# Kernel tuning notes

Hardware: AMD Instinct MI355X
Metric: run time of the kernel (lower is better)

Reference implementation:

```python
import jax, jax.numpy as jnp
import numpy as np

# Static graph-batch geometry: B graphs, N nodes each (contiguous), DEG avg degree.
B, N, DEG = 128, 512, 16
GID, GH = 128, 128      # g_in_dim, g_hidden_dim
CID, CE = 64, 64        # c_in_dim, c_embed_dim
HAZ = 256               # haz_dim
K1, K2, K3 = 256, 128, 64


def _gcn(x, src, dst, mask, W, b, n):
    # GCN layer with self loops over masked (surviving) nodes; masked-out nodes contribute nothing.
    h = x @ W  # [n, GH]
    w = mask[src] * mask[dst]                                  # edge alive iff both endpoints alive
    deg = mask + jax.ops.segment_sum(w, dst, num_segments=n)    # +mask = self loop
    dinv = jax.lax.rsqrt(jnp.maximum(deg, 1.0))
    norm = w * dinv[src] * dinv[dst]
    agg = jax.ops.segment_sum(norm[:, None] * h[src], dst, num_segments=n)
    self_term = h * (mask * dinv * dinv)[:, None]               # self-loop norm = 1/deg
    return (agg + self_term + b) * mask[:, None]


def _pool(x, mask, p, k):
    # Score-based top-k pooling (MVPool score -> gate -> keep top ratio per graph), mask-based for static shapes.
    score = jax.nn.sigmoid((x @ p) / jnp.sqrt(jnp.sum(p * p)))  # [B*N]
    s = jnp.where(mask > 0, score, -jnp.inf).reshape(B, N)
    _, idx = jax.lax.top_k(s, k)                                 # [B, k]
    new_mask = jnp.zeros((B, N), x.dtype).at[jnp.arange(B)[:, None], idx].set(1.0).reshape(-1)
    x = x * (score * new_mask)[:, None]
    return x, new_mask


def _readout(x, mask):
    # readout='both': concat(global_max_pool, global_mean_pool) per graph.
    xm = x.reshape(B, N, -1)
    m = mask.reshape(B, N, 1)
    mx = jnp.max(jnp.where(m > 0, xm, -1e30), axis=1)
    avg = jnp.sum(xm * m, axis=1) / jnp.maximum(jnp.sum(m, axis=1), 1.0)
    return jnp.concatenate([mx, avg], axis=1)


def _forward(x, inp_c, src, dst, W1, b1, W2, b2, W3, b3, p1, p2, p3, We, Wa, ba, Wb, bb, Wc):
    n = B * N
    mask = jnp.ones((n,), x.dtype)
    x = jax.nn.relu(_gcn(x, src, dst, mask, W1, b1, n))
    x, mask = _pool(x, mask, p1, K1)
    x1 = _readout(x, mask)
    x = jax.nn.relu(_gcn(x, src, dst, mask, W2, b2, n))
    x, mask = _pool(x, mask, p2, K2)
    x2 = _readout(x, mask)
    x = jax.nn.relu(_gcn(x, src, dst, mask, W3, b3, n))
    x, mask = _pool(x, mask, p3, K3)
    x3 = _readout(x, mask)
    hg = jax.nn.relu(x1) + jax.nn.relu(x2) + jax.nn.relu(x3)     # [B, 2*GH]
    embed = jax.nn.relu(inp_c @ We)                               # [B, CE]
    fusion = jnp.concatenate([embed, hg], axis=1)                 # [B, 320]
    h = jax.nn.relu(fusion @ Wa + ba)                             # dropout skipped (eval mode)
    h = jax.nn.relu(h @ Wb + bb)
    return h @ Wc                                                 # out_dim=1 -> Identity


def setup_inputs() -> dict:
    key = jax.random.key(0)
    ks = jax.random.split(key, 16)
    n = B * N
    x = jax.random.normal(ks[0], (n, GID), jnp.float32)
    inp_c = jax.random.normal(ks[1], (B, CID), jnp.float32)
    offs = (jnp.arange(B, dtype=jnp.int32) * N)[:, None]
    src = (jax.random.randint(ks[2], (B, N * DEG), 0, N, jnp.int32) + offs).reshape(-1)
    dst = (jax.random.randint(ks[3], (B, N * DEG), 0, N, jnp.int32) + offs).reshape(-1)
    edge_index = jnp.stack([src, dst])
    batch = jnp.arange(n, dtype=jnp.int32) // N
    def lin(k, i, o):
        return jax.random.normal(k, (i, o), jnp.float32) / np.float32(np.sqrt(i))
    return dict(
        x=x, inp_c=inp_c, edge_index=edge_index, batch=batch,
        W1=lin(ks[4], GID, GH), b1=jnp.zeros((GH,), jnp.float32),
        W2=lin(ks[5], GH, GH), b2=jnp.zeros((GH,), jnp.float32),
        W3=lin(ks[6], GH, GH), b3=jnp.zeros((GH,), jnp.float32),
        p1=jax.random.normal(ks[7], (GH,), jnp.float32),
        p2=jax.random.normal(ks[8], (GH,), jnp.float32),
        p3=jax.random.normal(ks[9], (GH,), jnp.float32),
        We=lin(ks[10], CID, CE),
        Wa=lin(ks[11], 2 * GH + CE, HAZ), ba=jnp.zeros((HAZ,), jnp.float32),
        Wb=lin(ks[12], HAZ, HAZ // 2), bb=jnp.zeros((HAZ // 2,), jnp.float32),
        Wc=lin(ks[13], HAZ // 2, 1),
    )


def reference(x, inp_c, edge_index, batch, W1, b1, W2, b2, W3, b3, p1, p2, p3, We, Wa, ba, Wb, bb, Wc):
    # batch is implicitly arange(n)//N (contiguous equal-size graphs); reductions use the reshape form.
    src, dst = edge_index[0], edge_index[1]
    return _forward(x, inp_c, src, dst, W1, b1, W2, b2, W3, b3, p1, p2, p3, We, Wa, ba, Wb, bb, Wc)
```

## Files before the change

### kernel.cpp

```cpp
#include <hip/hip_runtime.h>
#include <math.h>

#define NNODE 65536
#define NEDGE 1048576
#define NGRAPH 128
#define NPG 512
#define EPG 8192

typedef _Float16 f16x8 __attribute__((ext_vector_type(8)));
typedef _Float16 f16x4 __attribute__((ext_vector_type(4)));
typedef float f32x4 __attribute__((ext_vector_type(4)));


__global__ __launch_bounds__(512) void k_csr(const int* __restrict__ srcE, const int* __restrict__ dstE,
                                             int* __restrict__ rp, int* __restrict__ csr,
                                             float* __restrict__ gate, int* __restrict__ alive,
                                             float* __restrict__ dinv) {
    __shared__ int cnt[512];
    __shared__ int tmp[512];
    int g = blockIdx.x, t = threadIdx.x;
    int nd = g * NPG + t;
    cnt[t] = 0;
    gate[nd] = 1.f;
    alive[nd] = nd;
    __syncthreads();
    int ebase = g * EPG;
    int dl[16];
    for (int i = 0; i < 16; ++i) {
        int e = ebase + t + i * 512;
        int d = dstE[e] - g * NPG;
        dl[i] = d;
        atomicAdd(&cnt[d], 1);
    }
    __syncthreads();
    int v = cnt[t], incl = v;
    dinv[nd] = rsqrtf(1.f + (float)v);
    for (int off = 1; off < 512; off <<= 1) {
        tmp[t] = incl; __syncthreads();
        if (t >= off) incl += tmp[t - off];
        __syncthreads();
    }
    int excl = incl - v;
    rp[nd] = ebase + excl;
    if (g == NGRAPH - 1 && t == 511) rp[NNODE] = NEDGE;
    __syncthreads();
    cnt[t] = excl;
    __syncthreads();
    for (int i = 0; i < 16; ++i) {
        int e = ebase + t + i * 512;
        int pos = atomicAdd(&cnt[dl[i]], 1);
        csr[ebase + pos] = srcE[e];
    }
}


__global__ __launch_bounds__(256) void k_wconv(const float* __restrict__ W0, const float* __restrict__ W1,
                                               const float* __restrict__ W2, _Float16* __restrict__ wh,
                                               _Float16* __restrict__ wl) {
    int l = blockIdx.x >> 6;
    int e = (blockIdx.x & 63) * 256 + threadIdx.x;
    const float* W = (l == 0) ? W0 : (l == 1) ? W1 : W2;
    int k = e >> 7, n = e & 127;
    float w = W[e];
    _Float16 hi = (_Float16)w;
    _Float16 lo = (_Float16)((w - (float)hi) * 2048.0f);
    int nt = n >> 4, nn = n & 15, ks = k >> 5, quad = (k & 31) >> 3, j = k & 7;
    int off = l * 16384 + ((nt * 4 + ks) * 64 + (quad * 16 + nn)) * 8 + j;
    wh[off] = hi;
    wl[off] = lo;
}


#define CVT8(hi8, lo8, a0, a1, a2, a3, a4, a5, a6, a7)                         \
    {                                                                           \
        _Float16 q0 = (_Float16)a0, q1 = (_Float16)a1, q2 = (_Float16)a2,       \
                 q3 = (_Float16)a3, q4 = (_Float16)a4, q5 = (_Float16)a5,       \
                 q6 = (_Float16)a6, q7 = (_Float16)a7;                          \
        hi8 = (f16x8){q0, q1, q2, q3, q4, q5, q6, q7};                          \
        lo8 = (f16x8){(_Float16)((a0 - (float)q0) * 2048.f),                    \
                      (_Float16)((a1 - (float)q1) * 2048.f),                    \
                      (_Float16)((a2 - (float)q2) * 2048.f),                    \
                      (_Float16)((a3 - (float)q3) * 2048.f),                    \
                      (_Float16)((a4 - (float)q4) * 2048.f),                    \
                      (_Float16)((a5 - (float)q5) * 2048.f),                    \
                      (_Float16)((a6 - (float)q6) * 2048.f),                    \
                      (_Float16)((a7 - (float)q7) * 2048.f)};                   \
    }

__global__ __launch_bounds__(256, 2) void k_gemm(const float* __restrict__ x0, const _Float16* __restrict__ xh,
                                                 const _Float16* __restrict__ xl, const _Float16* __restrict__ wh,
                                                 const _Float16* __restrict__ wl, const float* __restrict__ gate,
                                                 const int* __restrict__ alive, float* __restrict__ h,
                                                 int srcF32) {
    __shared__ _Float16 aH[128 * 72];
    __shared__ _Float16 aL[128 * 72];
    __shared__ _Float16 bH[8192];
    __shared__ _Float16 bL[8192];
    int t = threadIdx.x;
    int lane = t & 63;
    int wv = t >> 6;
    int quad = lane >> 4, mm = lane & 15;
    int rowbase = blockIdx.x * 128;

    f32x4 accH[2][8], accM[2][8];
    for (int a = 0; a < 2; ++a)
        for (int b = 0; b < 8; ++b) {
            accH[a][b] = (f32x4){0.f, 0.f, 0.f, 0.f};
            accM[a][b] = (f32x4){0.f, 0.f, 0.f, 0.f};
        }

    for (int kh = 0; kh < 2; ++kh) {
        if (kh) __syncthreads();
        for (int pp = 0; pp < 4; ++pp) {
            int seg = t + pp * 256;
            int nt = seg >> 7, ksl = (seg >> 6) & 1, ln = seg & 63;
            int goff = ((nt * 4 + kh * 2 + ksl) * 64 + ln) * 8;
            *(uint4*)(bH + seg * 8) = *(const uint4*)(wh + goff);
            *(uint4*)(bL + seg * 8) = *(const uint4*)(wl + goff);
        }
        for (int pp = 0; pp < 4; ++pp) {
            int c = t + pp * 256;
            int r = c >> 3, ch = c & 7;
            int node = alive[rowbase + r];
            size_t src = (size_t)node * 128 + kh * 64 + ch * 8;
            f16x8 hi8, lo8;
            if (srcF32) {
                float4 v0 = *(const float4*)(x0 + src);
                float4 v1 = *(const float4*)(x0 + src + 4);
                CVT8(hi8, lo8, v0.x, v0.y, v0.z, v0.w, v1.x, v1.y, v1.z, v1.w);
            } else {
                hi8 = *(const f16x8*)(xh + src);
                lo8 = *(const f16x8*)(xl + src);
            }
            *(f16x8*)(aH + r * 72 + ch * 8) = hi8;
            *(f16x8*)(aL + r * 72 + ch * 8) = lo8;
        }
        __syncthreads();

        for (int ksl = 0; ksl < 2; ++ksl) {
            f16x8 Ah[2], Al[2];
            for (int mt = 0; mt < 2; ++mt) {
                int row = wv * 32 + mt * 16 + mm;
                Ah[mt] = *(const f16x8*)(aH + row * 72 + ksl * 32 + quad * 8);
                Al[mt] = *(const f16x8*)(aL + row * 72 + ksl * 32 + quad * 8);
            }
            for (int nt = 0; nt < 8; ++nt) {
                f16x8 Bh = *(const f16x8*)(bH + ((nt * 2 + ksl) * 64 + lane) * 8);
                f16x8 Bl = *(const f16x8*)(bL + ((nt * 2 + ksl) * 64 + lane) * 8);
                for (int mt = 0; mt < 2; ++mt) {
                    accH[mt][nt] = __builtin_amdgcn_mfma_f32_16x16x32_f16(Ah[mt], Bh, accH[mt][nt], 0, 0, 0);
                    accM[mt][nt] = __builtin_amdgcn_mfma_f32_16x16x32_f16(Ah[mt], Bl, accM[mt][nt], 0, 0, 0);
                    accM[mt][nt] = __builtin_amdgcn_mfma_f32_16x16x32_f16(Al[mt], Bh, accM[mt][nt], 0, 0, 0);
                }
            }
        }
    }

    for (int mt = 0; mt < 2; ++mt)
        for (int i = 0; i < 4; ++i) {
            int rl = wv * 32 + mt * 16 + quad * 4 + i;
            int node = alive[rowbase + rl];
            float g = gate[node];
            float* hr = h + (size_t)node * 128 + mm;
            for (int nt = 0; nt < 8; ++nt)
                hr[nt * 16] = g * (accH[mt][nt][i] + accM[mt][nt][i] * (1.f / 2048.f));
        }
}


__global__ __launch_bounds__(256) void k_agg(const float* __restrict__ h, const float* __restrict__ dinv,
                                             const int* __restrict__ rp, const int* __restrict__ csr,
                                             const int* __restrict__ alive, const float* __restrict__ bias,
                                             const float* __restrict__ p, _Float16* __restrict__ xh,
                                             _Float16* __restrict__ xl, float* __restrict__ score, int Kp) {
    __shared__ float2 nb[8][32];
    int t = threadIdx.x;
    int slot = t >> 5;
    int lane32 = t & 31;
    int half = slot & 1;
    int g = blockIdx.x & 127;
    int chunk = blockIdx.x >> 7;
    int idx = chunk * 8 + slot;

    int d = alive[g * Kp + idx];
    int jb = rp[d];
    int je = rp[d + 1];
    int deg = je - jb;

    int sid = 0; float wv = 0.f; bool livej = false;
    if (lane32 < deg) {
        sid = csr[jb + lane32];
        wv = dinv[sid];
        livej = (wv != 0.f);
    }
    unsigned long long bal = __ballot(livej);
    unsigned hm = (unsigned)(bal >> (half * 32));
    int cnt = __popc(hm);
    if (livej) {
        int pos = __popc(hm & ((1u << lane32) - 1));
        nb[slot][pos] = make_float2(wv, __int_as_float(sid));
    }

    float dvd = dinv[d];
    float4 hd = *(const float4*)(h + (size_t)d * 128 + lane32 * 4);
    float4 a0, a1, a2, a3;
    a0.x = dvd * hd.x; a0.y = dvd * hd.y; a0.z = dvd * hd.z; a0.w = dvd * hd.w;
    a1 = make_float4(0.f, 0.f, 0.f, 0.f);
    a2 = a1; a3 = a1;

    int j = 0;
    for (; j + 4 <= cnt; j += 4) {
        float2 n0 = nb[slot][j];
        float2 n1 = nb[slot][j + 1];
        float2 n2 = nb[slot][j + 2];
        float2 n3 = nb[slot][j + 3];
        float4 h0 = *(const float4*)(h + (size_t)__float_as_int(n0.y) * 128 + lane32 * 4);
        float4 h1 = *(const float4*)(h + (size_t)__float_as_int(n1.y) * 128 + lane32 * 4);
        float4 h2 = *(const float4*)(h + (size_t)__float_as_int(n2.y) * 128 + lane32 * 4);
        float4 h3 = *(const float4*)(h + (size_t)__float_as_int(n3.y) * 128 + lane32 * 4);
        a0.x = fmaf(n0.x, h0.x, a0.x); a0.y = fmaf(n0.x, h0.y, a0.y);
        a0.z = fmaf(n0.x, h0.z, a0.z); a0.w = fmaf(n0.x, h0.w, a0.w);
        a1.x = fmaf(n1.x, h1.x, a1.x); a1.y = fmaf(n1.x, h1.y, a1.y);
        a1.z = fmaf(n1.x, h1.z, a1.z); a1.w = fmaf(n1.x, h1.w, a1.w);
        a2.x = fmaf(n2.x, h2.x, a2.x); a2.y = fmaf(n2.x, h2.y, a2.y);
        a2.z = fmaf(n2.x, h2.z, a2.z); a2.w = fmaf(n2.x, h2.w, a2.w);
        a3.x = fmaf(n3.x, h3.x, a3.x); a3.y = fmaf(n3.x, h3.y, a3.y);
        a3.z = fmaf(n3.x, h3.z, a3.z); a3.w = fmaf(n3.x, h3.w, a3.w);
    }
    for (; j < cnt; ++j) {
        float2 n0 = nb[slot][j];
        float4 h0 = *(const float4*)(h + (size_t)__float_as_int(n0.y) * 128 + lane32 * 4);
        a0.x = fmaf(n0.x, h0.x, a0.x); a0.y = fmaf(n0.x, h0.y, a0.y);
        a0.z = fmaf(n0.x, h0.z, a0.z); a0.w = fmaf(n0.x, h0.w, a0.w);
    }
    for (int j2 = jb + 32; j2 < je; ++j2) {
        int s2 = csr[j2];
        float w2 = dinv[s2];
        float4 h2 = *(const float4*)(h + (size_t)s2 * 128 + lane32 * 4);
        a0.x = fmaf(w2, h2.x, a0.x); a0.y = fmaf(w2, h2.y, a0.y);
        a0.z = fmaf(w2, h2.z, a0.z); a0.w = fmaf(w2, h2.w, a0.w);
    }

    float4 b4 = *(const float4*)(bias + lane32 * 4);
    float4 o;
    o.x = fmaxf(fmaf(dvd, a0.x + a1.x + a2.x + a3.x, b4.x), 0.f);
    o.y = fmaxf(fmaf(dvd, a0.y + a1.y + a2.y + a3.y, b4.y), 0.f);
    o.z = fmaxf(fmaf(dvd, a0.z + a1.z + a2.z + a3.z, b4.z), 0.f);
    o.w = fmaxf(fmaf(dvd, a0.w + a1.w + a2.w + a3.w, b4.w), 0.f);

    _Float16 q0 = (_Float16)o.x, q1 = (_Float16)o.y, q2 = (_Float16)o.z, q3 = (_Float16)o.w;
    f16x4 oh = {q0, q1, q2, q3};
    f16x4 ol = {(_Float16)((o.x - (float)q0) * 2048.f), (_Float16)((o.y - (float)q1) * 2048.f),
                (_Float16)((o.z - (float)q2) * 2048.f), (_Float16)((o.w - (float)q3) * 2048.f)};
    *(f16x4*)(xh + (size_t)d * 128 + lane32 * 4) = oh;
    *(f16x4*)(xl + (size_t)d * 128 + lane32 * 4) = ol;

    float4 p4 = *(const float4*)(p + lane32 * 4);
    float ps = o.x * p4.x + o.y * p4.y + o.z * p4.z + o.w * p4.w;
    float q = p4.x * p4.x + p4.y * p4.y + p4.z * p4.z + p4.w * p4.w;
    for (int m = 16; m >= 1; m >>= 1) {
        ps += __shfl_xor(ps, m);
        q += __shfl_xor(q, m);
    }
    if (lane32 == 0) score[d] = 1.f / (1.f + expf(-ps * rsqrtf(q)));
}


__global__ __launch_bounds__(512) void k_pool(const _Float16* __restrict__ xh, const _Float16* __restrict__ xl,
                                              const float* __restrict__ score, float* __restrict__ gate,
                                              int* __restrict__ alive, float* __restrict__ hg,
                                              const int* __restrict__ rp, const int* __restrict__ csr,
                                              float* __restrict__ dinv, int K, int last) {
    __shared__ unsigned hist[1024];
    __shared__ unsigned wsum[8];
    __shared__ float cand[512];
    __shared__ int ad[256];
    __shared__ float ag[256];
    __shared__ float red[1024];
    __shared__ int m_new[512];
    __shared__ int scnt;
    __shared__ unsigned ccnt;
    __shared__ unsigned tbb, tbab;
    __shared__ float thrS;
    int t = threadIdx.x, g = blockIdx.x;
    int gbase = g * NPG;
    int d = gbase + t;

    float odv = dinv[d];
    int m = odv > 0.f;
    float sc = score[d];
    unsigned bits = m ? __float_as_uint(sc) : 0u;
    unsigned bucket = bits >> 21;
    hist[t] = 0; hist[t + 512] = 0;
    if (t == 0) { scnt = 0; ccnt = 0; }
    __syncthreads();
    atomicAdd(&hist[bucket], 1u);
    __syncthreads();
    unsigned a0 = hist[1023 - 2 * t];
    unsigned a1 = hist[1022 - 2 * t];
    unsigned pair = a0 + a1;
    unsigned v = pair;
    for (int o = 1; o < 64; o <<= 1) {
        unsigned n = __shfl_up(v, o);
        if ((t & 63) >= o) v += n;
    }
    if ((t & 63) == 63) wsum[t >> 6] = v;
    __syncthreads();
    if (t == 0) {
        unsigned run = 0;
        for (int i = 0; i < 8; ++i) { unsigned x = wsum[i]; wsum[i] = run; run += x; }
    }
    __syncthreads();
    unsigned incl = v + wsum[t >> 6];
    unsigned excl = incl - pair;
    unsigned uK = (unsigned)K;
    if (excl < uK && excl + a0 >= uK) { tbb = 1023 - 2 * t; tbab = excl; }
    else if (excl + a0 < uK && incl >= uK) { tbb = 1022 - 2 * t; tbab = excl + a0; }
    __syncthreads();
    unsigned bsel = tbb;
    unsigned r = uK - tbab;
    if (m && bucket == bsel) {
        unsigned pos = atomicAdd(&ccnt, 1u);
        cand[pos] = sc;
    }
    __syncthreads();
    unsigned c = ccnt;
    if (t < (int)c) {
        float vv = cand[t];
        unsigned gt = 0;
        for (unsigned i = 0; i < c; ++i) gt += (cand[i] > vv) ? 1u : 0u;
        if (gt == r - 1) thrS = vv;
    }
    __syncthreads();
    float thr = thrS;

    int nm = (m && sc >= thr) ? 1 : 0;
    gate[d] = nm ? sc : 0.f;
    m_new[t] = nm;
    if (nm) {
        int pos = atomicAdd(&scnt, 1);
        if (pos < K) {
            alive[g * K + pos] = d;
            ad[pos] = d;
            ag[pos] = sc;
        }
    }
    __syncthreads();

    if (!last) {
        float nd = 0.f;
        if (nm) {
            int jb = rp[d], je = rp[d + 1];
            int sum = 0;
            for (int j = jb; j < je; ++j) sum += m_new[csr[j] - gbase];
            nd = rsqrtf(1.f + (float)sum);
        }
        dinv[d] = nd;
    }

    int f = t & 127, c2 = t >> 7;
    float mx = 0.f, sm = 0.f;
#define REC(node) ((float)xh[(size_t)(node)*128 + f] + (float)xl[(size_t)(node)*128 + f] * (1.f / 2048.f))
    for (int j = c2; j < K; j += 16) {
        float v0 = REC(ad[j]) * ag[j];
        float v1 = REC(ad[j + 4]) * ag[j + 4];
        float v2 = REC(ad[j + 8]) * ag[j + 8];
        float v3 = REC(ad[j + 12]) * ag[j + 12];
        mx = fmaxf(fmaxf(fmaxf(mx, v0), fmaxf(v1, v2)), v3);
        sm += v0 + v1 + v2 + v3;
    }
#undef REC
    red[t] = mx; red[512 + t] = sm;
    __syncthreads();
    if (c2 == 0) {
        for (int cc = 1; cc < 4; ++cc) {
            mx = fmaxf(mx, red[cc * 128 + f]);
            sm += red[512 + cc * 128 + f];
        }
        hg[g * 256 + f] += mx;
        hg[g * 256 + 128 + f] += sm / (float)K;
    }
}


__global__ __launch_bounds__(256) void k_mlp(const float* __restrict__ inp_c, const float* __restrict__ hg,
                                             const float* __restrict__ We, const float* __restrict__ Wa,
                                             const float* __restrict__ ba, const float* __restrict__ Wb,
                                             const float* __restrict__ bb, const float* __restrict__ Wc,
                                             float* __restrict__ out) {
    __shared__ float fus[320];
    __shared__ float h1[256];
    __shared__ float h2[128];
    int t = threadIdx.x, g = blockIdx.x;
    if (t < 64) {
        float a = 0.f;
        for (int j = 0; j < 64; ++j) a = fmaf(inp_c[g * 64 + j], We[j * 64 + t], a);
        fus[t] = fmaxf(a, 0.f);
    }
    fus[64 + t] = hg[g * 256 + t];
    __syncthreads();
    {
        float a = ba[t];
        for (int j = 0; j < 320; ++j) a = fmaf(fus[j], Wa[j * 256 + t], a);
        h1[t] = fmaxf(a, 0.f);
    }
    __syncthreads();
    if (t < 128) {
        float a = bb[t];
        for (int j = 0; j < 256; ++j) a = fmaf(h1[j], Wb[j * 128 + t], a);
        h2[t] = fmaxf(a, 0.f);
    }
    __syncthreads();
    if (t == 0) {
        float a = 0.f;
        for (int j = 0; j < 128; ++j) a = fmaf(h2[j], Wc[j], a);
        out[g] = a;
    }
}


extern "C" void kernel_launch(void* const* d_in, const int* in_sizes, int n_in,
                              void* d_out, int out_size, void* d_ws, size_t ws_size,
                              hipStream_t stream) {
    (void)in_sizes; (void)n_in; (void)out_size; (void)ws_size;
    const float* x_in  = (const float*)d_in[0];
    const float* inp_c = (const float*)d_in[1];
    const int*   ei    = (const int*)d_in[2];
    const int* srcE = ei;
    const int* dstE = ei + NEDGE;
    const float* Wl[3] = {(const float*)d_in[4], (const float*)d_in[6], (const float*)d_in[8]};
    const float* bl[3] = {(const float*)d_in[5], (const float*)d_in[7], (const float*)d_in[9]};
    const float* Pl[3] = {(const float*)d_in[10], (const float*)d_in[11], (const float*)d_in[12]};
    const float* We = (const float*)d_in[13];
    const float* Wa = (const float*)d_in[14];
    const float* ba = (const float*)d_in[15];
    const float* Wb = (const float*)d_in[16];
    const float* bb = (const float*)d_in[17];
    const float* Wc = (const float*)d_in[18];
    float* out = (float*)d_out;

    char* w = (char*)d_ws;
    size_t off = 0;
    auto alloc = [&](size_t bytes) -> void* {
        void* p = w + off;
        off = (off + bytes + 255) & ~(size_t)255;
        return p;
    };
    int*   rp    = (int*)alloc((NNODE + 1) * 4);
    int*   csr   = (int*)alloc(NEDGE * 4);
    float* dinv  = (float*)alloc(NNODE * 4);
    float* gate  = (float*)alloc(NNODE * 4);
    float* score = (float*)alloc(NNODE * 4);
    int*   alive = (int*)alloc(NNODE * 4);
    float* hbuf  = (float*)alloc((size_t)NNODE * 128 * 4);
    _Float16* xh = (_Float16*)alloc((size_t)NNODE * 128 * 2);
    _Float16* xl = (_Float16*)alloc((size_t)NNODE * 128 * 2);
    float* hg    = (float*)alloc(NGRAPH * 256 * 4);
    _Float16* wfh = (_Float16*)alloc(3 * 16384 * 2);
    _Float16* wfl = (_Float16*)alloc(3 * 16384 * 2);

    hipMemsetAsync(hg, 0, NGRAPH * 256 * 4, stream);
    k_wconv<<<192, 256, 0, stream>>>(Wl[0], Wl[1], Wl[2], wfh, wfl);
    k_csr<<<NGRAPH, 512, 0, stream>>>(srcE, dstE, rp, csr, gate, alive, dinv);

    const int rows_in[3] = {65536, 32768, 16384};
    const int Ks[3] = {256, 128, 64};
    const int Kp[3] = {512, 256, 128};
    for (int l = 0; l < 3; ++l) {
        k_gemm<<<rows_in[l] / 128, 256, 0, stream>>>(x_in, xh, xl, wfh + l * 16384, wfl + l * 16384,
                                                     gate, alive, hbuf, l == 0);
        k_agg<<<rows_in[l] / 8, 256, 0, stream>>>(hbuf, dinv, rp, csr, alive, bl[l], Pl[l],
                                                  xh, xl, score, Kp[l]);
        k_pool<<<NGRAPH, 512, 0, stream>>>(xh, xl, score, gate, alive, hg,
                                           rp, csr, dinv, Ks[l], l == 2);
    }
    k_mlp<<<NGRAPH, 256, 0, stream>>>(inp_c, hg, We, Wa, ba, Wb, bb, Wc, out);
}
```

Baseline: 291.1 us.

## Split each node's neighbor aggregation across two half-waves and reduce via shuffle

The aggregation kernel now assigns one full 64-lane wave per destination node instead of one 32-lane half-wave. The live neighbors are interleaved between the two halves and padded to a multiple of four with a zero-weight self entry, and each half accumulates its share. The two partial sums are combined with a cross-half shuffle, and the gather loop is unrolled by eight. This doubles the block count and raises memory-level parallelism per node, at the cost of half the lanes doing redundant epilogue work and extra padded loads.

```diff
diff --git a/kernel.cpp b/kernel.cpp
--- a/kernel.cpp
+++ b/kernel.cpp
@@ -168,92 +168,120 @@
 }
 
 
+#define FMA4(wt, hv, acc)                      \
+    {                                          \
+        acc.x = fmaf(wt, hv.x, acc.x);         \
+        acc.y = fmaf(wt, hv.y, acc.y);         \
+        acc.z = fmaf(wt, hv.z, acc.z);         \
+        acc.w = fmaf(wt, hv.w, acc.w);         \
+    }
+
 __global__ __launch_bounds__(256) void k_agg(const float* __restrict__ h, const float* __restrict__ dinv,
                                              const int* __restrict__ rp, const int* __restrict__ csr,
                                              const int* __restrict__ alive, const float* __restrict__ bias,
                                              const float* __restrict__ p, _Float16* __restrict__ xh,
                                              _Float16* __restrict__ xl, float* __restrict__ score, int Kp) {
-    __shared__ float2 nb[8][32];
+    __shared__ float2 nb[4][2][32];
     int t = threadIdx.x;
-    int slot = t >> 5;
+    int wv = t >> 6;
+    int lane = t & 63;
     int lane32 = t & 31;
-    int half = slot & 1;
+    int half = (t >> 5) & 1;
     int g = blockIdx.x & 127;
     int chunk = blockIdx.x >> 7;
-    int idx = chunk * 8 + slot;
+    int idx = chunk * 4 + wv;
 
     int d = alive[g * Kp + idx];
     int jb = rp[d];
     int je = rp[d + 1];
     int deg = je - jb;
 
-    int sid = 0; float wv = 0.f; bool livej = false;
-    if (lane32 < deg) {
-        sid = csr[jb + lane32];
-        wv = dinv[sid];
-        livej = (wv != 0.f);
+    nb[wv][half][lane32] = make_float2(0.f, __int_as_float(d));
+
+    int sid = 0;
+    float wvv = 0.f;
+    bool livej = false;
+    if (lane < deg) {
+        sid = csr[jb + lane];
+        wvv = dinv[sid];
+        livej = (wvv != 0.f);
     }
     unsigned long long bal = __ballot(livej);
-    unsigned hm = (unsigned)(bal >> (half * 32));
-    int cnt = __popc(hm);
+    int cnt = __popcll(bal);
     if (livej) {
-        int pos = __popc(hm & ((1u << lane32) - 1));
-        nb[slot][pos] = make_float2(wv, __int_as_float(sid));
-    }
+        int pos = __popcll(bal & ((1ull << lane) - 1ull));
+        nb[wv][pos & 1][pos >> 1] = make_float2(wvv, __int_as_float(sid));
+    }
+
+    int cg = half ? (cnt >> 1) : ((cnt + 1) >> 1);
+    int c4 = (cg + 3) & ~3;
 
     float dvd = dinv[d];
     float4 hd = *(const float4*)(h + (size_t)d * 128 + lane32 * 4);
+    float sw = half ? 0.f : dvd;
     float4 a0, a1, a2, a3;
-    a0.x = dvd * hd.x; a0.y = dvd * hd.y; a0.z = dvd * hd.z; a0.w = dvd * hd.w;
+    a0.x = sw * hd.x; a0.y = sw * hd.y; a0.z = sw * hd.z; a0.w = sw * hd.w;
     a1 = make_float4(0.f, 0.f, 0.f, 0.f);
     a2 = a1; a3 = a1;
 
+    const float2* nbp = &nb[wv][half][0];
     int j = 0;
-    for (; j + 4 <= cnt; j += 4) {
-        float2 n0 = nb[slot][j];
-        float2 n1 = nb[slot][j + 1];
-        float2 n2 = nb[slot][j + 2];
-        float2 n3 = nb[slot][j + 3];
+    for (; j + 8 <= c4; j += 8) {
+        float2 n0 = nbp[j + 0], n1 = nbp[j + 1], n2 = nbp[j + 2], n3 = nbp[j + 3];
+        float2 n4 = nbp[j + 4], n5 = nbp[j + 5], n6 = nbp[j + 6], n7 = nbp[j + 7];
         float4 h0 = *(const float4*)(h + (size_t)__float_as_int(n0.y) * 128 + lane32 * 4);
         float4 h1 = *(const float4*)(h + (size_t)__float_as_int(n1.y) * 128 + lane32 * 4);
         float4 h2 = *(const float4*)(h + (size_t)__float_as_int(n2.y) * 128 + lane32 * 4);
         float4 h3 = *(const float4*)(h + (size_t)__float_as_int(n3.y) * 128 + lane32 * 4);
-        a0.x = fmaf(n0.x, h0.x, a0.x); a0.y = fmaf(n0.x, h0.y, a0.y);
-        a0.z = fmaf(n0.x, h0.z, a0.z); a0.w = fmaf(n0.x, h0.w, a0.w);
-        a1.x = fmaf(n1.x, h1.x, a1.x); a1.y = fmaf(n1.x, h1.y, a1.y);
-        a1.z = fmaf(n1.x, h1.z, a1.z); a1.w = fmaf(n1.x, h1.w, a1.w);
-        a2.x = fmaf(n2.x, h2.x, a2.x); a2.y = fmaf(n2.x, h2.y, a2.y);
-        a2.z = fmaf(n2.x, h2.z, a2.z); a2.w = fmaf(n2.x, h2.w, a2.w);
-        a3.x = fmaf(n3.x, h3.x, a3.x); a3.y = fmaf(n3.x, h3.y, a3.y);
-        a3.z = fmaf(n3.x, h3.z, a3.z); a3.w = fmaf(n3.x, h3.w, a3.w);
-    }
-    for (; j < cnt; ++j) {
-        float2 n0 = nb[slot][j];
+        float4 h4 = *(const float4*)(h + (size_t)__float_as_int(n4.y) * 128 + lane32 * 4);
+        float4 h5 = *(const float4*)(h + (size_t)__float_as_int(n5.y) * 128 + lane32 * 4);
+        float4 h6 = *(const float4*)(h + (size_t)__float_as_int(n6.y) * 128 + lane32 * 4);
+        float4 h7 = *(const float4*)(h + (size_t)__float_as_int(n7.y) * 128 + lane32 * 4);
+        FMA4(n0.x, h0, a0); FMA4(n1.x, h1, a1); FMA4(n2.x, h2, a2); FMA4(n3.x, h3, a3);
+        FMA4(n4.x, h4, a0); FMA4(n5.x, h5, a1); FMA4(n6.x, h6, a2); FMA4(n7.x, h7, a3);
+    }
+    if (j < c4) {
+        float2 n0 = nbp[j + 0], n1 = nbp[j + 1], n2 = nbp[j + 2], n3 = nbp[j + 3];
         float4 h0 = *(const float4*)(h + (size_t)__float_as_int(n0.y) * 128 + lane32 * 4);
-        a0.x = fmaf(n0.x, h0.x, a0.x); a0.y = fmaf(n0.x, h0.y, a0.y);
-        a0.z = fmaf(n0.x, h0.z, a0.z); a0.w = fmaf(n0.x, h0.w, a0.w);
-    }
-    for (int j2 = jb + 32; j2 < je; ++j2) {
-        int s2 = csr[j2];
-        float w2 = dinv[s2];
-        float4 h2 = *(const float4*)(h + (size_t)s2 * 128 + lane32 * 4);
-        a0.x = fmaf(w2, h2.x, a0.x); a0.y = fmaf(w2, h2.y, a0.y);
-        a0.z = fmaf(w2, h2.z, a0.z); a0.w = fmaf(w2, h2.w, a0.w);
-    }
+        float4 h1 = *(const float4*)(h + (size_t)__float_as_int(n1.y) * 128 + lane32 * 4);
+        float4 h2 = *(const float4*)(h + (size_t)__float_as_int(n2.y) * 128 + lane32 * 4);
+        float4 h3 = *(const float4*)(h + (size_t)__float_as_int(n3.y) * 128 + lane32 * 4);
+        FMA4(n0.x, h0, a0); FMA4(n1.x, h1, a1); FMA4(n2.x, h2, a2); FMA4(n3.x, h3, a3);
+    }
+    if (half == 0) {
+        for (int j2 = jb + 64; j2 < je; ++j2) {
+            int s2 = csr[j2];
+            float w2 = dinv[s2];
+            float4 h2 = *(const float4*)(h + (size_t)s2 * 128 + lane32 * 4);
+            FMA4(w2, h2, a0);
+        }
+    }
+
+    float4 s;
+    s.x = a0.x + a1.x + a2.x + a3.x;
+    s.y = a0.y + a1.y + a2.y + a3.y;
+    s.z = a0.z + a1.z + a2.z + a3.z;
+    s.w = a0.w + a1.w + a2.w + a3.w;
+    s.x += __shfl_xor(s.x, 32);
+    s.y += __shfl_xor(s.y, 32);
+    s.z += __shfl_xor(s.z, 32);
+    s.w += __shfl_xor(s.w, 32);
 
     float4 b4 = *(const float4*)(bias + lane32 * 4);
     float4 o;
-    o.x = fmaxf(fmaf(dvd, a0.x + a1.x + a2.x + a3.x, b4.x), 0.f);
-    o.y = fmaxf(fmaf(dvd, a0.y + a1.y + a2.y + a3.y, b4.y), 0.f);
-    o.z = fmaxf(fmaf(dvd, a0.z + a1.z + a2.z + a3.z, b4.z), 0.f);
-    o.w = fmaxf(fmaf(dvd, a0.w + a1.w + a2.w + a3.w, b4.w), 0.f);
-
-    _Float16 q0 = (_Float16)o.x, q1 = (_Float16)o.y, q2 = (_Float16)o.z, q3 = (_Float16)o.w;
-    f16x4 oh = {q0, q1, q2, q3};
-    f16x4 ol = {(_Float16)((o.x - (float)q0) * 2048.f), (_Float16)((o.y - (float)q1) * 2048.f),
-                (_Float16)((o.z - (float)q2) * 2048.f), (_Float16)((o.w - (float)q3) * 2048.f)};
-    *(f16x4*)(xh + (size_t)d * 128 + lane32 * 4) = oh;
-    *(f16x4*)(xl + (size_t)d * 128 + lane32 * 4) = ol;
+    o.x = fmaxf(fmaf(dvd, s.x, b4.x), 0.f);
+    o.y = fmaxf(fmaf(dvd, s.y, b4.y), 0.f);
+    o.z = fmaxf(fmaf(dvd, s.z, b4.z), 0.f);
+    o.w = fmaxf(fmaf(dvd, s.w, b4.w), 0.f);
+
+    if (half == 0) {
+        _Float16 q0 = (_Float16)o.x, q1 = (_Float16)o.y, q2 = (_Float16)o.z, q3 = (_Float16)o.w;
+        f16x4 oh = {q0, q1, q2, q3};
+        f16x4 ol = {(_Float16)((o.x - (float)q0) * 2048.f), (_Float16)((o.y - (float)q1) * 2048.f),
+                    (_Float16)((o.z - (float)q2) * 2048.f), (_Float16)((o.w - (float)q3) * 2048.f)};
+        *(f16x4*)(xh + (size_t)d * 128 + lane32 * 4) = oh;
+        *(f16x4*)(xl + (size_t)d * 128 + lane32 * 4) = ol;
+    }
 
     float4 p4 = *(const float4*)(p + lane32 * 4);
     float ps = o.x * p4.x + o.y * p4.y + o.z * p4.z + o.w * p4.w;
@@ -262,7 +290,7 @@
         ps += __shfl_xor(ps, m);
         q += __shfl_xor(q, m);
     }
-    if (lane32 == 0) score[d] = 1.f / (1.f + expf(-ps * rsqrtf(q)));
+    if (lane == 0) score[d] = 1.f / (1.f + expf(-ps * rsqrtf(q)));
 }
 
 
@@ -469,7 +497,7 @@
     for (int l = 0; l < 3; ++l) {
         k_gemm<<<rows_in[l] / 128, 256, 0, stream>>>(x_in, xh, xl, wfh + l * 16384, wfl + l * 16384,
                                                      gate, alive, hbuf, l == 0);
-        k_agg<<<rows_in[l] / 8, 256, 0, stream>>>(hbuf, dinv, rp, csr, alive, bl[l], Pl[l],
+        k_agg<<<rows_in[l] / 4, 256, 0, stream>>>(hbuf, dinv, rp, csr, alive, bl[l], Pl[l],
                                                   xh, xl, score, Kp[l]);
         k_pool<<<NGRAPH, 512, 0, stream>>>(xh, xl, score, gate, alive, hg,
                                            rp, csr, dinv, Ks[l], l == 2);
```

Measured after the change: 299.9 us. 3.0% more time.
